# Kernel tuning notes

Measured on AMD Instinct MI355X. Metric: run time of the kernel, lower is better.

## Reference

```python
import jax, jax.numpy as jnp
import numpy as np

EPS = 1e-5

def _bn(x, p):
    # eval-mode BatchNorm over the last (channel) axis; p = [gamma, beta, mean, var]
    g, b, m, v = p[0], p[1], p[2], p[3]
    return (x - m) * jax.lax.rsqrt(v + EPS) * g + b

def _mk_bn(key, c):
    kg, kb, km, kv = jax.random.split(key, 4)
    return jnp.stack([
        jax.random.uniform(kg, (c,), minval=0.5, maxval=1.5),
        jax.random.normal(kb, (c,)) * 0.1,
        jax.random.normal(km, (c,)) * 0.1,
        jax.random.uniform(kv, (c,), minval=0.5, maxval=1.5),
    ]).astype(jnp.float32)

def setup_inputs() -> dict:
    key = jax.random.key(0)
    ks = jax.random.split(key, 12)
    B, N, K = 2, 65536, 16
    IN_CH, OUT_CH = 32, 128
    D = IN_CH + 3            # 35
    C16 = OUT_CH // 16       # 8
    C4 = OUT_CH // 4         # 32
    G = 1                    # num_group
    feats = jax.random.normal(ks[0], (B, N, D), dtype=jnp.float32)
    idx = jax.random.randint(ks[1], (B, N, K), 0, N, dtype=jnp.int64)
    s = lambda fi, fo: (2.0 / fi) ** 0.5
    return {
        "features": feats,
        "idx": idx,
        "point_W": jax.random.normal(ks[2], (10, C16), dtype=jnp.float32) * s(10, C16),
        "point_bn": _mk_bn(ks[3], C16),
        "eta_W": jax.random.normal(ks[4], (IN_CH, C16), dtype=jnp.float32) * s(IN_CH, C16),
        "eta_bn": _mk_bn(ks[5], C16),
        "mu_W": jax.random.normal(ks[6], (IN_CH, C16), dtype=jnp.float32) * s(IN_CH, C16),
        "mu_bn": _mk_bn(ks[7], C16),
        "gamma_W": jax.random.normal(ks[8], (D, C4), dtype=jnp.float32) * s(D, C4),
        "gamma_bn": _mk_bn(ks[9], C4),
        "map_W": jax.random.normal(ks[10], (3 * C16, G), dtype=jnp.float32) * s(3 * C16, G),
        "map_bn": _mk_bn(ks[10], G),
        "fc_W": jax.random.normal(ks[11], (C4, OUT_CH), dtype=jnp.float32) * s(C4, OUT_CH),
    }

def reference(features, idx, point_W, point_bn, eta_W, eta_bn, mu_W, mu_bn,
              gamma_W, gamma_bn, map_W, map_bn, fc_W):
    # features: [B,N,D] (D = 3 xyz + in_channel), idx: [B,N,K] kNN indices
    nbr = jax.vmap(lambda f, i: f[i])(features, idx)     # [B,N,K,D] gather
    pn = nbr[..., :3]                                    # neighbor xyz
    pnf = nbr[..., 3:]                                   # neighbor feats
    feat = features[..., 3:]                             # center feats [B,N,Cin]
    p = features[:, :, None, :3]                         # center xyz, bcast over K
    diff = p - pn
    point = jnp.concatenate([
        jnp.sum(diff * diff, axis=-1, keepdims=True),
        jnp.broadcast_to(p, pn.shape), pn, diff,
    ], axis=-1)                                          # [B,N,K,10]
    point = jax.nn.relu(_bn(point @ point_W, point_bn))  # [B,N,K,C16]
    eta = _bn((feat @ eta_W)[:, :, None, :], eta_bn)     # [B,N,1,C16] (repeat over K)
    mu = _bn(pnf @ mu_W, mu_bn)                          # [B,N,K,C16]
    feature = jnp.concatenate([jnp.broadcast_to(eta, mu.shape), mu], axis=-1)  # concat mode
    feature = jnp.concatenate([point, feature], axis=-1)                       # [B,N,K,3*C16]
    feature = jax.nn.relu(_bn(feature @ map_W, map_bn))  # [B,N,K,G]
    gam = _bn(nbr @ gamma_W, gamma_bn)                   # [B,N,K,C4]
    rep = gam.shape[-1] // feature.shape[-1]             # out/4 / num_group
    feature = jnp.tile(feature, (1, 1, 1, rep))          # channel repeat
    out = jnp.max(feature * gam, axis=2)                 # max over neighbors -> [B,N,C4]
    return out @ fc_W                                    # [B,N,out_channel]
```

## Files before the change

kernel.cpp:

```cpp
#include <hip/hip_runtime.h>
#include <hip/hip_fp16.h>
#include <math.h>

#define N_PTS   65536
#define BATCH   2
#define TOTAL   (BATCH * N_PTS)
#define NPACK_DW 16
#define CPACK   12
#define EPSB    1e-5f

typedef float  f32x4  __attribute__((ext_vector_type(4)));
typedef _Float16 f16x8 __attribute__((ext_vector_type(8)));

static __device__ inline unsigned h2u(float a, float b) {
    __half2 h = __floats2half2_rn(a, b);
    union { __half2 h; unsigned u; } cv; cv.h = h; return cv.u;
}
static __device__ inline float2 u2f2(unsigned u) {
    union { unsigned u; __half2 h; } cv; cv.u = u; return __half22float2(cv.h);
}
static __device__ inline unsigned pk_max(unsigned a, unsigned b) {
    unsigned r; asm("v_pk_max_f16 %0, %1, %2" : "=v"(r) : "v"(a), "v"(b)); return r;
}

__global__ __launch_bounds__(256) void k1_precompute(
    const float* __restrict__ feats,
    const float* __restrict__ pW,
    const float* __restrict__ pBN,
    const float* __restrict__ eW,
    const float* __restrict__ eBN,
    const float* __restrict__ mW,
    const float* __restrict__ mBN,
    const float* __restrict__ gW,
    const float* __restrict__ gBN,
    const float* __restrict__ mapW,
    unsigned* __restrict__ packN,
    float* __restrict__ packC)
{
    __shared__ float sG[35 * 32];
    __shared__ float sE[32 * 8];
    __shared__ float sM[32 * 8];
    __shared__ float sF[256 * 35];

    const int tid = threadIdx.x;
    const int base = blockIdx.x * 256;

    for (int i = tid; i < 35 * 32; i += 256) sG[i] = gW[i];
    sE[tid] = eW[tid]; sM[tid] = mW[tid];
#pragma unroll
    for (int t = 0; t < 35; ++t)
        sF[t * 256 + tid] = feats[(size_t)base * 35 + t * 256 + tid];
    __syncthreads();

    const float* f = sF + tid * 35;
    const float x = f[0], y = f[1], z = f[2];
    const float pp = x * x + y * y + z * z;

    float G[32];
#pragma unroll
    for (int q = 0; q < 32; ++q) G[q] = 0.f;
#pragma unroll 4
    for (int d = 0; d < 35; ++d) {
        const float fd = f[d];
        const float4* w4 = (const float4*)(sG + d * 32);
#pragma unroll
        for (int q4 = 0; q4 < 8; ++q4) {
            const float4 w = w4[q4];
            G[q4 * 4 + 0] = fmaf(fd, w.x, G[q4 * 4 + 0]);
            G[q4 * 4 + 1] = fmaf(fd, w.y, G[q4 * 4 + 1]);
            G[q4 * 4 + 2] = fmaf(fd, w.z, G[q4 * 4 + 2]);
            G[q4 * 4 + 3] = fmaf(fd, w.w, G[q4 * 4 + 3]);
        }
    }
#pragma unroll
    for (int q = 0; q < 32; ++q) {
        const float g = gBN[q], b = gBN[32 + q], m = gBN[64 + q], v = gBN[96 + q];
        const float s = g / sqrtf(v + EPSB);
        G[q] = fmaf(G[q], s, b - m * s);
    }

    float eta[8], mu[8];
#pragma unroll
    for (int q = 0; q < 8; ++q) { eta[q] = 0.f; mu[q] = 0.f; }
#pragma unroll 4
    for (int i = 0; i < 32; ++i) {
        const float fi = f[3 + i];
        const float4* e4 = (const float4*)(sE + i * 8);
        const float4* m4 = (const float4*)(sM + i * 8);
#pragma unroll
        for (int h = 0; h < 2; ++h) {
            const float4 we = e4[h], wm = m4[h];
            eta[h * 4 + 0] = fmaf(fi, we.x, eta[h * 4 + 0]);
            eta[h * 4 + 1] = fmaf(fi, we.y, eta[h * 4 + 1]);
            eta[h * 4 + 2] = fmaf(fi, we.z, eta[h * 4 + 2]);
            eta[h * 4 + 3] = fmaf(fi, we.w, eta[h * 4 + 3]);
            mu[h * 4 + 0] = fmaf(fi, wm.x, mu[h * 4 + 0]);
            mu[h * 4 + 1] = fmaf(fi, wm.y, mu[h * 4 + 1]);
            mu[h * 4 + 2] = fmaf(fi, wm.z, mu[h * 4 + 2]);
            mu[h * 4 + 3] = fmaf(fi, wm.w, mu[h * 4 + 3]);
        }
    }
    float etadot = 0.f, Mdot = 0.f;
#pragma unroll
    for (int q = 0; q < 8; ++q) {
        const float ge = eBN[q], be = eBN[8 + q], me = eBN[16 + q], ve = eBN[24 + q];
        const float se = ge / sqrtf(ve + EPSB);
        etadot = fmaf(fmaf(eta[q], se, be - me * se), mapW[8 + q], etadot);
        const float gm = mBN[q], bm = mBN[8 + q], mm = mBN[16 + q], vm = mBN[24 + q];
        const float sm = gm / sqrtf(vm + EPSB);
        Mdot = fmaf(fmaf(mu[q], sm, bm - mm * sm), mapW[16 + q], Mdot);
    }

    float Bnp[8], Ap[8];
#pragma unroll
    for (int q = 0; q < 8; ++q) {
        const float pw0 = pW[q];
        const float g = pBN[q], b = pBN[8 + q], m = pBN[16 + q], v = pBN[24 + q];
        const float s = g / sqrtf(v + EPSB);
        const float t = b - m * s;
        const float Braw = pp * pw0
            + x * (pW[32 + q] - pW[56 + q])
            + y * (pW[40 + q] - pW[64 + q])
            + z * (pW[48 + q] - pW[72 + q]);
        const float Araw = pp * pw0
            + x * (pW[8 + q]  + pW[56 + q])
            + y * (pW[16 + q] + pW[64 + q])
            + z * (pW[24 + q] + pW[72 + q]);
        Bnp[q] = Braw * s;
        Ap[q]  = fmaf(Araw, s, t);
    }

    const int j = base + tid;
    float gmax = 0.f;
#pragma unroll
    for (int q = 0; q < 32; ++q) gmax = fmaxf(gmax, fabsf(G[q]));
    const float inv = (gmax > 0.f) ? (127.f / gmax) : 0.f;
    unsigned gq[8];
#pragma unroll
    for (int qd = 0; qd < 8; ++qd) {
        unsigned d = 0;
#pragma unroll
        for (int b = 0; b < 4; ++b) {
            const int q8 = (int)rintf(G[4 * qd + b] * inv) + 128;
            d |= ((unsigned)q8 & 0xffu) << (8 * b);
        }
        gq[qd] = d;
    }
    union { float f; unsigned u; } sc; sc.f = gmax;

    uint4* PN = (uint4*)(packN + (size_t)j * NPACK_DW);
    PN[0] = make_uint4(h2u(x, y), h2u(z, Mdot), h2u(Bnp[0], Bnp[1]), h2u(Bnp[2], Bnp[3]));
    PN[1] = make_uint4(h2u(Bnp[4], Bnp[5]), h2u(Bnp[6], Bnp[7]), gq[0], gq[1]);
    PN[2] = make_uint4(gq[2], gq[3], gq[4], gq[5]);
    PN[3] = make_uint4(gq[6], gq[7], sc.u, 0u);

    float4* PC = (float4*)(packC + (size_t)j * CPACK);
    PC[0] = make_float4(x, y, z, etadot);
    PC[1] = make_float4(Ap[0], Ap[1], Ap[2], Ap[3]);
    PC[2] = make_float4(Ap[4], Ap[5], Ap[6], Ap[7]);
}

__global__ __launch_bounds__(256) void k2_aggregate_fc(
    const int* __restrict__ idx,
    const unsigned* __restrict__ packN,
    const float* __restrict__ packC,
    const float* __restrict__ pW,
    const float* __restrict__ pBN,
    const float* __restrict__ mapW,
    const float* __restrict__ mapBN,
    const float* __restrict__ fcW,
    float* __restrict__ out)
{
    __shared__ __align__(16) unsigned short sPool[32 * 40];

    const int bid  = blockIdx.x;
    const int xcd  = bid & 7, slot = bid >> 3;
    const int cb   = (xcd < 4) ? (slot * 4 + xcd)
                               : (2048 + slot * 4 + (xcd - 4));
    const int cbase = cb * 32;

    const int tid  = threadIdx.x;
    const int cl   = tid >> 3;
    const int ks   = tid & 7;
    const int c    = cbase + cl;
    const int lane = tid & 63;
    const int w    = tid >> 6;
    const int lm   = lane & 15, lq = lane >> 4;

    f16x8 bfrag[2];
#pragma unroll
    for (int ntj = 0; ntj < 2; ++ntj) {
        const int nt = 2 * w + ntj;
        union { unsigned short u[8]; f16x8 v; } cv;
#pragma unroll
        for (int j = 0; j < 8; ++j)
            cv.u[j] = __half_as_ushort(__float2half_rn(fcW[(8 * lq + j) * 128 + nt * 16 + lm]));
        bfrag[ntj] = cv.v;
    }

    float ms, mt;
    {
        const float g = mapBN[0], b = mapBN[1], m = mapBN[2], v = mapBN[3];
        ms = g / sqrtf(v + EPSB);
        mt = b - m * ms;
    }
    float W0p[8], mW0[8];
#pragma unroll
    for (int q = 0; q < 8; ++q) {
        const float g = pBN[q], v = pBN[24 + q];
        const float s = g / sqrtf(v + EPSB);
        W0p[q] = 2.f * pW[q] * s;
        mW0[q] = mapW[q];
    }

    const float4* PC = (const float4*)(packC + (size_t)c * CPACK);
    const float4 c0 = PC[0], c1 = PC[1], c2 = PC[2];
    const float px = c0.x, py = c0.y, pz = c0.z, etadot = c0.w;
    const float Ap[8] = { c1.x, c1.y, c1.z, c1.w, c2.x, c2.y, c2.z, c2.w };

    const int2 ib2 = ((const int2*)idx)[c * 8 + ks];
    const int bbase = c & ~(N_PTS - 1);

    unsigned o16[16];
#pragma unroll
    for (int q = 0; q < 16; ++q) o16[q] = 0xFC00FC00u;

    const uint4* P0 = (const uint4*)(packN + (size_t)(bbase + ib2.x) * NPACK_DW);
    const uint4* P1 = (const uint4*)(packN + (size_t)(bbase + ib2.y) * NPACK_DW);
    uint4 n0[4] = { P0[0], P0[1], P0[2], P0[3] };
    uint4 n1[4] = { P1[0], P1[1], P1[2], P1[3] };

#pragma unroll
    for (int k = 0; k < 2; ++k) {
        const uint4* N = k ? n1 : n0;
        const float2 xy = u2f2(N[0].x), zM = u2f2(N[0].y);
        const float dot3 = px * xy.x + py * xy.y + pz * zM.x;

        const unsigned bn[4] = { N[0].z, N[0].w, N[1].x, N[1].y };
        float pd = 0.f;
#pragma unroll
        for (int q = 0; q < 4; ++q) {
            const float2 bn2 = u2f2(bn[q]);
            const float u0 = Ap[2 * q]     + bn2.x - dot3 * W0p[2 * q];
            const float u1 = Ap[2 * q + 1] + bn2.y - dot3 * W0p[2 * q + 1];
            pd = fmaf(fmaxf(u0, 0.f), mW0[2 * q], pd);
            pd = fmaf(fmaxf(u1, 0.f), mW0[2 * q + 1], pd);
        }
        float s = fmaf(pd + etadot + zM.y, ms, mt);
        s = fmaxf(s, 0.f);

        union { unsigned u; float f; } sc; sc.u = N[3].z;
        const float t  = s * sc.f * (1.f / 127.f);
        const float nt = -128.f * t;

        const unsigned gd[8] = { N[1].z, N[1].w, N[2].x, N[2].y,
                                 N[2].z, N[2].w, N[3].x, N[3].y };
#pragma unroll
        for (int qd = 0; qd < 8; ++qd) {
            const unsigned dwv = gd[qd];
            const float v0 = fmaf(t, (float)( dwv        & 0xffu), nt);
            const float v1 = fmaf(t, (float)((dwv >>  8) & 0xffu), nt);
            const float v2 = fmaf(t, (float)((dwv >> 16) & 0xffu), nt);
            const float v3 = fmaf(t, (float)( dwv >> 24        ), nt);
            o16[2 * qd]     = pk_max(o16[2 * qd],     h2u(v0, v1));
            o16[2 * qd + 1] = pk_max(o16[2 * qd + 1], h2u(v2, v3));
        }
    }

#pragma unroll
    for (int q = 0; q < 16; ++q) {
        unsigned v = o16[q];
        v = pk_max(v, (unsigned)__shfl_xor((int)v, 1));
        v = pk_max(v, (unsigned)__shfl_xor((int)v, 2));
        v = pk_max(v, (unsigned)__shfl_xor((int)v, 4));
        o16[q] = v;
    }

    {
        uint2 pk;
        pk.x = o16[2 * ks];
        pk.y = o16[2 * ks + 1];
        *(uint2*)(sPool + cl * 40 + ks * 4) = pk;
    }
    __syncthreads();

    f32x4 acc[2][2];
#pragma unroll
    for (int a = 0; a < 2; ++a)
#pragma unroll
        for (int b = 0; b < 2; ++b)
            acc[a][b] = (f32x4){0.f, 0.f, 0.f, 0.f};

#pragma unroll
    for (int mtile = 0; mtile < 2; ++mtile) {
        const f16x8 afrag = *(const f16x8*)(sPool + (mtile * 16 + lm) * 40 + lq * 8);
#pragma unroll
        for (int ntj = 0; ntj < 2; ++ntj)
            acc[mtile][ntj] = __builtin_amdgcn_mfma_f32_16x16x32_f16(
                afrag, bfrag[ntj], acc[mtile][ntj], 0, 0, 0);
    }

#pragma unroll
    for (int mtile = 0; mtile < 2; ++mtile)
#pragma unroll
        for (int ntj = 0; ntj < 2; ++ntj) {
            const int nt = 2 * w + ntj;
#pragma unroll
            for (int r = 0; r < 4; ++r)
                __builtin_nontemporal_store(acc[mtile][ntj][r],
                    &out[(size_t)(cbase + mtile * 16 + lq * 4 + r) * 128 + nt * 16 + lm]);
        }
}

extern "C" void kernel_launch(void* const* d_in, const int* in_sizes, int n_in,
                              void* d_out, int out_size, void* d_ws, size_t ws_size,
                              hipStream_t stream) {
    const float* feats    = (const float*)d_in[0];
    const int*   idx      = (const int*)  d_in[1];
    const float* point_W  = (const float*)d_in[2];
    const float* point_bn = (const float*)d_in[3];
    const float* eta_W    = (const float*)d_in[4];
    const float* eta_bn   = (const float*)d_in[5];
    const float* mu_W     = (const float*)d_in[6];
    const float* mu_bn    = (const float*)d_in[7];
    const float* gamma_W  = (const float*)d_in[8];
    const float* gamma_bn = (const float*)d_in[9];
    const float* map_W    = (const float*)d_in[10];
    const float* map_bn   = (const float*)d_in[11];
    const float* fc_W     = (const float*)d_in[12];
    float* out = (float*)d_out;

    unsigned* packN = (unsigned*)d_ws;
    float*    packC = (float*)(packN + (size_t)TOTAL * NPACK_DW);

    hipLaunchKernelGGL(k1_precompute, dim3(TOTAL / 256), dim3(256), 0, stream,
                       feats, point_W, point_bn, eta_W, eta_bn, mu_W, mu_bn,
                       gamma_W, gamma_bn, map_W, packN, packC);
    hipLaunchKernelGGL(k2_aggregate_fc, dim3(TOTAL / 32), dim3(256), 0, stream,
                       idx, packN, packC, point_W, point_bn, map_W, map_bn,
                       fc_W, out);
}
```

Baseline: 161.5 us.

## Dequantize int8 gamma with packed f16 FMA and hoist constants into precompute kernel

The aggregation kernel now dequantizes int8 gamma values with a magic-number trick: each byte is OR'd into the f16 exponent pattern 0x6400, then a single packed f16 FMA applies scale and offset, replacing per-byte float conversions, FMAs and pack conversions. To make this work, the precompute kernel reorders the bytes within each dword. The precompute kernel also processes two points per thread with 128-thread blocks, loads features as float4, and writes fp16 fc weight fragments and gate constants once, so the aggregation kernel no longer recomputes them per block. The f16 FMA runs with less precision than the fp32 math it replaces, and round-toward-zero packing of the scale adds more error.

Result: slower. 167.8 us (+3.9%).

```diff
diff --git a/kernel.cpp b/kernel.cpp
--- a/kernel.cpp
+++ b/kernel.cpp
@@ -22,8 +22,14 @@
 static __device__ inline unsigned pk_max(unsigned a, unsigned b) {
     unsigned r; asm("v_pk_max_f16 %0, %1, %2" : "=v"(r) : "v"(a), "v"(b)); return r;
 }
-
-__global__ __launch_bounds__(256) void k1_precompute(
+static __device__ inline unsigned pk_fma(unsigned a, unsigned b, unsigned c) {
+    unsigned r; asm("v_pk_fma_f16 %0, %1, %2, %3" : "=v"(r) : "v"(a), "v"(b), "v"(c)); return r;
+}
+static __device__ inline unsigned pkrtz(float a, float b) {
+    unsigned r; asm("v_cvt_pkrtz_f16_f32 %0, %1, %2" : "=v"(r) : "v"(a), "v"(b)); return r;
+}
+
+__global__ __launch_bounds__(128) void k1_precompute(
     const float* __restrict__ feats,
     const float* __restrict__ pW,
     const float* __restrict__ pBN,
@@ -34,141 +40,183 @@
     const float* __restrict__ gW,
     const float* __restrict__ gBN,
     const float* __restrict__ mapW,
+    const float* __restrict__ mapBN,
+    const float* __restrict__ fcW,
     unsigned* __restrict__ packN,
-    float* __restrict__ packC)
+    float* __restrict__ packC,
+    unsigned* __restrict__ fc16,
+    float* __restrict__ gateC)
 {
+    __shared__ float sF[256 * 35];
     __shared__ float sG[35 * 32];
     __shared__ float sE[32 * 8];
     __shared__ float sM[32 * 8];
-    __shared__ float sF[256 * 35];
 
     const int tid = threadIdx.x;
     const int base = blockIdx.x * 256;
 
-    for (int i = tid; i < 35 * 32; i += 256) sG[i] = gW[i];
-    sE[tid] = eW[tid]; sM[tid] = mW[tid];
-#pragma unroll
-    for (int t = 0; t < 35; ++t)
-        sF[t * 256 + tid] = feats[(size_t)base * 35 + t * 256 + tid];
+    {
+        const float4* src4 = (const float4*)(feats + (size_t)base * 35);
+        float4* dst4 = (float4*)sF;
+        for (int i = tid; i < 2240; i += 128) dst4[i] = src4[i];
+        for (int i = tid; i < 1120; i += 128) sG[i] = gW[i];
+        sE[tid] = eW[tid]; sE[tid + 128] = eW[tid + 128];
+        sM[tid] = mW[tid]; sM[tid + 128] = mW[tid + 128];
+    }
     __syncthreads();
 
-    const float* f = sF + tid * 35;
-    const float x = f[0], y = f[1], z = f[2];
-    const float pp = x * x + y * y + z * z;
-
-    float G[32];
-#pragma unroll
-    for (int q = 0; q < 32; ++q) G[q] = 0.f;
-#pragma unroll 4
+    const float* f0 = sF + tid * 35;
+    const float* f1 = sF + (tid + 128) * 35;
+
+    float G[2][32];
+#pragma unroll
+    for (int q = 0; q < 32; ++q) { G[0][q] = 0.f; G[1][q] = 0.f; }
+#pragma unroll 5
     for (int d = 0; d < 35; ++d) {
-        const float fd = f[d];
+        const float fd0 = f0[d], fd1 = f1[d];
         const float4* w4 = (const float4*)(sG + d * 32);
 #pragma unroll
         for (int q4 = 0; q4 < 8; ++q4) {
             const float4 w = w4[q4];
-            G[q4 * 4 + 0] = fmaf(fd, w.x, G[q4 * 4 + 0]);
-            G[q4 * 4 + 1] = fmaf(fd, w.y, G[q4 * 4 + 1]);
-            G[q4 * 4 + 2] = fmaf(fd, w.z, G[q4 * 4 + 2]);
-            G[q4 * 4 + 3] = fmaf(fd, w.w, G[q4 * 4 + 3]);
-        }
-    }
-#pragma unroll
-    for (int q = 0; q < 32; ++q) {
-        const float g = gBN[q], b = gBN[32 + q], m = gBN[64 + q], v = gBN[96 + q];
-        const float s = g / sqrtf(v + EPSB);
-        G[q] = fmaf(G[q], s, b - m * s);
-    }
-
-    float eta[8], mu[8];
-#pragma unroll
-    for (int q = 0; q < 8; ++q) { eta[q] = 0.f; mu[q] = 0.f; }
+            G[0][q4 * 4 + 0] = fmaf(fd0, w.x, G[0][q4 * 4 + 0]);
+            G[0][q4 * 4 + 1] = fmaf(fd0, w.y, G[0][q4 * 4 + 1]);
+            G[0][q4 * 4 + 2] = fmaf(fd0, w.z, G[0][q4 * 4 + 2]);
+            G[0][q4 * 4 + 3] = fmaf(fd0, w.w, G[0][q4 * 4 + 3]);
+            G[1][q4 * 4 + 0] = fmaf(fd1, w.x, G[1][q4 * 4 + 0]);
+            G[1][q4 * 4 + 1] = fmaf(fd1, w.y, G[1][q4 * 4 + 1]);
+            G[1][q4 * 4 + 2] = fmaf(fd1, w.z, G[1][q4 * 4 + 2]);
+            G[1][q4 * 4 + 3] = fmaf(fd1, w.w, G[1][q4 * 4 + 3]);
+        }
+    }
+
+    float eta[2][8], mu[2][8];
+#pragma unroll
+    for (int q = 0; q < 8; ++q) { eta[0][q]=0.f; eta[1][q]=0.f; mu[0][q]=0.f; mu[1][q]=0.f; }
 #pragma unroll 4
     for (int i = 0; i < 32; ++i) {
-        const float fi = f[3 + i];
+        const float fi0 = f0[3 + i], fi1 = f1[3 + i];
         const float4* e4 = (const float4*)(sE + i * 8);
         const float4* m4 = (const float4*)(sM + i * 8);
 #pragma unroll
         for (int h = 0; h < 2; ++h) {
             const float4 we = e4[h], wm = m4[h];
-            eta[h * 4 + 0] = fmaf(fi, we.x, eta[h * 4 + 0]);
-            eta[h * 4 + 1] = fmaf(fi, we.y, eta[h * 4 + 1]);
-            eta[h * 4 + 2] = fmaf(fi, we.z, eta[h * 4 + 2]);
-            eta[h * 4 + 3] = fmaf(fi, we.w, eta[h * 4 + 3]);
-            mu[h * 4 + 0] = fmaf(fi, wm.x, mu[h * 4 + 0]);
-            mu[h * 4 + 1] = fmaf(fi, wm.y, mu[h * 4 + 1]);
-            mu[h * 4 + 2] = fmaf(fi, wm.z, mu[h * 4 + 2]);
-            mu[h * 4 + 3] = fmaf(fi, wm.w, mu[h * 4 + 3]);
-        }
-    }
-    float etadot = 0.f, Mdot = 0.f;
-#pragma unroll
-    for (int q = 0; q < 8; ++q) {
-        const float ge = eBN[q], be = eBN[8 + q], me = eBN[16 + q], ve = eBN[24 + q];
-        const float se = ge / sqrtf(ve + EPSB);
-        etadot = fmaf(fmaf(eta[q], se, be - me * se), mapW[8 + q], etadot);
-        const float gm = mBN[q], bm = mBN[8 + q], mm = mBN[16 + q], vm = mBN[24 + q];
-        const float sm = gm / sqrtf(vm + EPSB);
-        Mdot = fmaf(fmaf(mu[q], sm, bm - mm * sm), mapW[16 + q], Mdot);
-    }
-
-    float Bnp[8], Ap[8];
-#pragma unroll
-    for (int q = 0; q < 8; ++q) {
-        const float pw0 = pW[q];
-        const float g = pBN[q], b = pBN[8 + q], m = pBN[16 + q], v = pBN[24 + q];
-        const float s = g / sqrtf(v + EPSB);
-        const float t = b - m * s;
-        const float Braw = pp * pw0
-            + x * (pW[32 + q] - pW[56 + q])
-            + y * (pW[40 + q] - pW[64 + q])
-            + z * (pW[48 + q] - pW[72 + q]);
-        const float Araw = pp * pw0
-            + x * (pW[8 + q]  + pW[56 + q])
-            + y * (pW[16 + q] + pW[64 + q])
-            + z * (pW[24 + q] + pW[72 + q]);
-        Bnp[q] = Braw * s;
-        Ap[q]  = fmaf(Araw, s, t);
-    }
-
-    const int j = base + tid;
-    float gmax = 0.f;
-#pragma unroll
-    for (int q = 0; q < 32; ++q) gmax = fmaxf(gmax, fabsf(G[q]));
-    const float inv = (gmax > 0.f) ? (127.f / gmax) : 0.f;
-    unsigned gq[8];
-#pragma unroll
-    for (int qd = 0; qd < 8; ++qd) {
-        unsigned d = 0;
-#pragma unroll
-        for (int b = 0; b < 4; ++b) {
-            const int q8 = (int)rintf(G[4 * qd + b] * inv) + 128;
-            d |= ((unsigned)q8 & 0xffu) << (8 * b);
-        }
-        gq[qd] = d;
-    }
-    union { float f; unsigned u; } sc; sc.f = gmax;
-
-    uint4* PN = (uint4*)(packN + (size_t)j * NPACK_DW);
-    PN[0] = make_uint4(h2u(x, y), h2u(z, Mdot), h2u(Bnp[0], Bnp[1]), h2u(Bnp[2], Bnp[3]));
-    PN[1] = make_uint4(h2u(Bnp[4], Bnp[5]), h2u(Bnp[6], Bnp[7]), gq[0], gq[1]);
-    PN[2] = make_uint4(gq[2], gq[3], gq[4], gq[5]);
-    PN[3] = make_uint4(gq[6], gq[7], sc.u, 0u);
-
-    float4* PC = (float4*)(packC + (size_t)j * CPACK);
-    PC[0] = make_float4(x, y, z, etadot);
-    PC[1] = make_float4(Ap[0], Ap[1], Ap[2], Ap[3]);
-    PC[2] = make_float4(Ap[4], Ap[5], Ap[6], Ap[7]);
+#pragma unroll
+            for (int b = 0; b < 4; ++b) {
+                const float ew = (&we.x)[b], mw = (&wm.x)[b];
+                eta[0][h*4+b] = fmaf(fi0, ew, eta[0][h*4+b]);
+                eta[1][h*4+b] = fmaf(fi1, ew, eta[1][h*4+b]);
+                mu[0][h*4+b]  = fmaf(fi0, mw, mu[0][h*4+b]);
+                mu[1][h*4+b]  = fmaf(fi1, mw, mu[1][h*4+b]);
+            }
+        }
+    }
+
+#pragma unroll
+    for (int pt = 0; pt < 2; ++pt) {
+        const float* f = pt ? f1 : f0;
+        const int j = base + tid + pt * 128;
+        const float x = f[0], y = f[1], z = f[2];
+        const float pp = x * x + y * y + z * z;
+
+        float Gp[32];
+#pragma unroll
+        for (int q = 0; q < 32; ++q) {
+            const float g = gBN[q], b = gBN[32 + q], m = gBN[64 + q], v = gBN[96 + q];
+            const float s = g / sqrtf(v + EPSB);
+            Gp[q] = fmaf(G[pt][q], s, b - m * s);
+        }
+
+        float etadot = 0.f, Mdot = 0.f;
+#pragma unroll
+        for (int q = 0; q < 8; ++q) {
+            const float ge = eBN[q], be = eBN[8 + q], me = eBN[16 + q], ve = eBN[24 + q];
+            const float se = ge / sqrtf(ve + EPSB);
+            etadot = fmaf(fmaf(eta[pt][q], se, be - me * se), mapW[8 + q], etadot);
+            const float gm = mBN[q], bm = mBN[8 + q], mm = mBN[16 + q], vm = mBN[24 + q];
+            const float sm = gm / sqrtf(vm + EPSB);
+            Mdot = fmaf(fmaf(mu[pt][q], sm, bm - mm * sm), mapW[16 + q], Mdot);
+        }
+
+        float Bnp[8], Ap[8];
+#pragma unroll
+        for (int q = 0; q < 8; ++q) {
+            const float pw0 = pW[q];
+            const float g = pBN[q], b = pBN[8 + q], m = pBN[16 + q], v = pBN[24 + q];
+            const float s = g / sqrtf(v + EPSB);
+            const float t = b - m * s;
+            const float Braw = pp * pw0
+                + x * (pW[32 + q] - pW[56 + q])
+                + y * (pW[40 + q] - pW[64 + q])
+                + z * (pW[48 + q] - pW[72 + q]);
+            const float Araw = pp * pw0
+                + x * (pW[8 + q]  + pW[56 + q])
+                + y * (pW[16 + q] + pW[64 + q])
+                + z * (pW[24 + q] + pW[72 + q]);
+            Bnp[q] = Braw * s;
+            Ap[q]  = fmaf(Araw, s, t);
+        }
+
+        float gmax = 0.f;
+#pragma unroll
+        for (int q = 0; q < 32; ++q) gmax = fmaxf(gmax, fabsf(Gp[q]));
+        const float inv = (gmax > 0.f) ? (127.f / gmax) : 0.f;
+        unsigned gq[8];
+#pragma unroll
+        for (int qd = 0; qd < 8; ++qd) {
+            const unsigned u0 = (unsigned)((int)rintf(Gp[4*qd+0] * inv) + 128) & 0xffu;
+            const unsigned u1 = (unsigned)((int)rintf(Gp[4*qd+1] * inv) + 128) & 0xffu;
+            const unsigned u2 = (unsigned)((int)rintf(Gp[4*qd+2] * inv) + 128) & 0xffu;
+            const unsigned u3 = (unsigned)((int)rintf(Gp[4*qd+3] * inv) + 128) & 0xffu;
+            gq[qd] = u0 | (u2 << 8) | (u1 << 16) | (u3 << 24);
+        }
+        union { float f; unsigned u; } sc; sc.f = gmax;
+
+        uint4* PN = (uint4*)(packN + (size_t)j * NPACK_DW);
+        PN[0] = make_uint4(h2u(x, y), h2u(z, Mdot), h2u(Bnp[0], Bnp[1]), h2u(Bnp[2], Bnp[3]));
+        PN[1] = make_uint4(h2u(Bnp[4], Bnp[5]), h2u(Bnp[6], Bnp[7]), gq[0], gq[1]);
+        PN[2] = make_uint4(gq[2], gq[3], gq[4], gq[5]);
+        PN[3] = make_uint4(gq[6], gq[7], sc.u, 0u);
+
+        float4* PC = (float4*)(packC + (size_t)j * CPACK);
+        PC[0] = make_float4(x, y, z, etadot);
+        PC[1] = make_float4(Ap[0], Ap[1], Ap[2], Ap[3]);
+        PC[2] = make_float4(Ap[4], Ap[5], Ap[6], Ap[7]);
+    }
+
+    if (blockIdx.x == 0) {
+        for (int fi = tid; fi < 512; fi += 128) {
+            const int lm = fi & 15, nt = (fi >> 4) & 7, lq = fi >> 7;
+            unsigned dws[4];
+#pragma unroll
+            for (int p = 0; p < 4; ++p) {
+                const float a = fcW[(8 * lq + 2 * p)     * 128 + nt * 16 + lm];
+                const float b = fcW[(8 * lq + 2 * p + 1) * 128 + nt * 16 + lm];
+                dws[p] = h2u(a, b);
+            }
+            ((uint4*)fc16)[fi] = make_uint4(dws[0], dws[1], dws[2], dws[3]);
+        }
+        if (tid == 0) {
+#pragma unroll
+            for (int q = 0; q < 8; ++q) {
+                const float g = pBN[q], v = pBN[24 + q];
+                const float s = g / sqrtf(v + EPSB);
+                gateC[q]     = 2.f * pW[q] * s;
+                gateC[8 + q] = mapW[q];
+            }
+            const float g = mapBN[0], b = mapBN[1], m = mapBN[2], v = mapBN[3];
+            const float ms = g / sqrtf(v + EPSB);
+            gateC[16] = ms;
+            gateC[17] = b - m * ms;
+        }
+    }
 }
 
 __global__ __launch_bounds__(256) void k2_aggregate_fc(
     const int* __restrict__ idx,
     const unsigned* __restrict__ packN,
     const float* __restrict__ packC,
-    const float* __restrict__ pW,
-    const float* __restrict__ pBN,
-    const float* __restrict__ mapW,
-    const float* __restrict__ mapBN,
-    const float* __restrict__ fcW,
+    const unsigned* __restrict__ fc16,
+    const float* __restrict__ gateC,
     float* __restrict__ out)
 {
     __shared__ __align__(16) unsigned short sPool[32 * 40];
@@ -190,28 +238,15 @@
     f16x8 bfrag[2];
 #pragma unroll
     for (int ntj = 0; ntj < 2; ++ntj) {
-        const int nt = 2 * w + ntj;
-        union { unsigned short u[8]; f16x8 v; } cv;
-#pragma unroll
-        for (int j = 0; j < 8; ++j)
-            cv.u[j] = __half_as_ushort(__float2half_rn(fcW[(8 * lq + j) * 128 + nt * 16 + lm]));
+        union { uint4 u4; f16x8 v; } cv;
+        cv.u4 = ((const uint4*)fc16)[(lq * 8 + 2 * w + ntj) * 16 + lm];
         bfrag[ntj] = cv.v;
     }
 
-    float ms, mt;
-    {
-        const float g = mapBN[0], b = mapBN[1], m = mapBN[2], v = mapBN[3];
-        ms = g / sqrtf(v + EPSB);
-        mt = b - m * ms;
-    }
+    const float ms = gateC[16], mt = gateC[17];
     float W0p[8], mW0[8];
 #pragma unroll
-    for (int q = 0; q < 8; ++q) {
-        const float g = pBN[q], v = pBN[24 + q];
-        const float s = g / sqrtf(v + EPSB);
-        W0p[q] = 2.f * pW[q] * s;
-        mW0[q] = mapW[q];
-    }
+    for (int q = 0; q < 8; ++q) { W0p[q] = gateC[q]; mW0[q] = gateC[8 + q]; }
 
     const float4* PC = (const float4*)(packC + (size_t)c * CPACK);
     const float4 c0 = PC[0], c1 = PC[1], c2 = PC[2];
@@ -250,20 +285,20 @@
         s = fmaxf(s, 0.f);
 
         union { unsigned u; float f; } sc; sc.u = N[3].z;
-        const float t  = s * sc.f * (1.f / 127.f);
-        const float nt = -128.f * t;
+        const float t = s * sc.f * (1.f / 127.f);
+        const unsigned t2 = pkrtz(t, t);
+        const float d = -1152.f * t;
+        const unsigned d2 = pkrtz(d, d);
 
         const unsigned gd[8] = { N[1].z, N[1].w, N[2].x, N[2].y,
                                  N[2].z, N[2].w, N[3].x, N[3].y };
 #pragma unroll
         for (int qd = 0; qd < 8; ++qd) {
             const unsigned dwv = gd[qd];
-            const float v0 = fmaf(t, (float)( dwv        & 0xffu), nt);
-            const float v1 = fmaf(t, (float)((dwv >>  8) & 0xffu), nt);
-            const float v2 = fmaf(t, (float)((dwv >> 16) & 0xffu), nt);
-            const float v3 = fmaf(t, (float)( dwv >> 24        ), nt);
-            o16[2 * qd]     = pk_max(o16[2 * qd],     h2u(v0, v1));
-            o16[2 * qd + 1] = pk_max(o16[2 * qd + 1], h2u(v2, v3));
+            const unsigned lo = (dwv & 0x00FF00FFu) | 0x64006400u;
+            const unsigned hi = ((dwv >> 8) & 0x00FF00FFu) | 0x64006400u;
+            o16[2 * qd]     = pk_max(o16[2 * qd],     pk_fma(lo, t2, d2));
+            o16[2 * qd + 1] = pk_max(o16[2 * qd + 1], pk_fma(hi, t2, d2));
         }
     }
 
@@ -332,11 +367,13 @@
 
     unsigned* packN = (unsigned*)d_ws;
     float*    packC = (float*)(packN + (size_t)TOTAL * NPACK_DW);
-
-    hipLaunchKernelGGL(k1_precompute, dim3(TOTAL / 256), dim3(256), 0, stream,
+    unsigned* fc16  = (unsigned*)(packC + (size_t)TOTAL * CPACK);
+    float*    gateC = (float*)(fc16 + 2048);
+
+    hipLaunchKernelGGL(k1_precompute, dim3(TOTAL / 256), dim3(128), 0, stream,
                        feats, point_W, point_bn, eta_W, eta_bn, mu_W, mu_bn,
-                       gamma_W, gamma_bn, map_W, packN, packC);
+                       gamma_W, gamma_bn, map_W, map_bn, fc_W,
+                       packN, packC, fc16, gateC);
     hipLaunchKernelGGL(k2_aggregate_fc, dim3(TOTAL / 32), dim3(256), 0, stream,
-                       idx, packN, packC, point_W, point_bn, map_W, map_bn,
-                       fc_W, out);
-}
+                       idx, packN, packC, fc16, gateC, out);
+}
```
